# Performance work log

Hardware: AMD Instinct MI355X
Metric: run time of the kernel (lower is better)

## Reference

```python
import itertools
import jax, jax.numpy as jnp
import numpy as np

B = 1024      # graphs
N = 40        # atoms per graph (module supports 1..49)
ETA = 64
K = 32        # num_clusters
ZD = 32       # z_dim
NA = 10       # num_atom_types
NB = 5        # num_bond_types + 1
CH, AH, BH = 128, 128, 64
TAU = 1.0


def _resblock(x, W1, b1, W2, b2, Ws, bs):
    # assumed ResidualBlock: Linear->ReLU->(dropout, eval=identity)->Linear + linear skip
    h = jax.nn.relu(x @ W1 + b1)
    return h @ W2 + b2 + (x @ Ws + bs)


def setup_inputs() -> dict:
    key = jax.random.key(0)
    ks = jax.random.split(key, 24)
    s = 0.05
    pairs = np.array(list(itertools.combinations(range(N), 2)), dtype=np.int32)  # [780,2]
    offsets = (np.arange(B, dtype=np.int32) * N)[:, None, None]
    edge_index = jnp.asarray((pairs[None] + offsets).reshape(-1, 2))  # [B*780, 2]
    return {
        "eta": jax.random.normal(ks[0], (B, ETA), jnp.float32),
        "gumbel_noise": jax.random.gumbel(ks[1], (B * N, K), jnp.float32),
        "z_noise": jax.random.normal(ks[2], (B * N, ZD), jnp.float32),
        "cW1": jax.random.normal(ks[3], (ETA, CH)) * s, "cb1": jnp.zeros((CH,)),
        "cW2": jax.random.normal(ks[4], (CH, K)) * s, "cb2": jnp.zeros((K,)),
        "cWs": jax.random.normal(ks[5], (ETA, K)) * s, "cbs": jnp.zeros((K,)),
        "cluster_means": jax.random.normal(ks[6], (K, ZD)),
        "cluster_log_sigmas": jnp.full((K, ZD), -2.0),
        "aW1": jax.random.normal(ks[7], (ZD, AH)) * s, "ab1": jnp.zeros((AH,)),
        "aW2": jax.random.normal(ks[8], (AH, NA)) * s, "ab2": jnp.zeros((NA,)),
        "aWs": jax.random.normal(ks[9], (ZD, NA)) * s, "abs_": jnp.zeros((NA,)),
        "bond_matrix": jax.random.normal(ks[10], (NB, ZD, ZD)),
        "bW1": jax.random.normal(ks[11], (NB, BH)) * s, "bb1": jnp.zeros((BH,)),
        "bW2": jax.random.normal(ks[12], (BH, NB)) * s, "bb2": jnp.zeros((NB,)),
        "bWs": jax.random.normal(ks[13], (NB, NB)) * s, "bbs": jnp.zeros((NB,)),
        "edge_index": edge_index,
    }


def reference(eta, gumbel_noise, z_noise,
              cW1, cb1, cW2, cb2, cWs, cbs,
              cluster_means, cluster_log_sigmas,
              aW1, ab1, aW2, ab2, aWs, abs_,
              bond_matrix, bW1, bb1, bW2, bb2, bWs, bbs,
              edge_index):
    # decode_eta: mixture weights
    pi = jax.nn.softmax(_resblock(eta, cW1, cb1, cW2, cb2, cWs, cbs), axis=1)  # [B,K]
    log_pi = jnp.log(pi)
    # sample_c: gumbel-softmax (hard, straight-through) per node
    logits = jnp.repeat(log_pi, N, axis=0)                      # [B*N, K]
    y_soft = jax.nn.softmax((logits + gumbel_noise) / TAU, axis=-1)
    y_hard = jax.nn.one_hot(jnp.argmax(y_soft, axis=-1), K, dtype=y_soft.dtype)
    c = y_hard + y_soft - jax.lax.stop_gradient(y_soft)         # straight-through
    # sample_z
    mu = c @ cluster_means                                      # [B*N, ZD]
    log_sigma = c @ cluster_log_sigmas
    sigma = jnp.exp(jnp.clip(log_sigma, -20.0, 30.0))
    z = z_noise * sigma + mu
    # decode_z: atom logits
    atom_types = _resblock(z, aW1, ab1, aW2, ab2, aWs, abs_)    # [B*N, NA]
    # symmetrized per-bond-type bilinear form over edge node pairs
    Wsym = 0.5 * (bond_matrix + jnp.swapaxes(bond_matrix, 1, 2))  # [NB, ZD, ZD]
    zi = z[edge_index[:, 0]]                                    # [E, ZD]
    zj = z[edge_index[:, 1]]                                    # [E, ZD]
    bil = jnp.einsum('ed,tdc,ec->et', zi, Wsym, zj)             # [E, NB]
    edge_logits = _resblock(bil, bW1, bb1, bW2, bb2, bWs, bbs)
    edge_types = jax.nn.softmax(edge_logits, axis=1)            # [E, NB]
    return atom_types, edge_types
```

## Files before the change

kernel.cpp:

```cpp
#include <hip/hip_runtime.h>

constexpr int NPAIR = 780;

constexpr int OFF_ZT = 0;
constexpr int OFF_A  = 1280;
constexpr int UTP    = 1280;
constexpr int OFF_BT = 5120;
constexpr int SH_TOT = 9020;

__global__ __launch_bounds__(256) void prep_kernel(
    const float* __restrict__ eta,
    const float* __restrict__ cW1, const float* __restrict__ cb1,
    const float* __restrict__ cW2, const float* __restrict__ cb2,
    const float* __restrict__ cWs, const float* __restrict__ cbs,
    const float* __restrict__ bond, const float* __restrict__ lsig,
    const float* __restrict__ bW1, const float* __restrict__ bb1,
    const float* __restrict__ bW2, const float* __restrict__ bb2,
    const float* __restrict__ bWs, const float* __restrict__ bbs,
    float* __restrict__ log_pi, float* __restrict__ wsym,
    float* __restrict__ sigma, float* __restrict__ hwg)
{
  if (blockIdx.x < 256) {
    const int lane = threadIdx.x & 63, wid = threadIdx.x >> 6;
    const int row = blockIdx.x * 4 + wid;
    __shared__ __align__(16) float etas[4][64];
    __shared__ __align__(16) float hs[4][128];
    etas[wid][lane] = eta[row * 64 + lane];
    __syncthreads();
    float a0 = cb1[lane], a1 = cb1[lane + 64];
    for (int d = 0; d < 64; ++d) {
      float ed = etas[wid][d];
      a0 += ed * cW1[d * 128 + lane];
      a1 += ed * cW1[d * 128 + lane + 64];
    }
    hs[wid][lane] = fmaxf(a0, 0.f);
    hs[wid][lane + 64] = fmaxf(a1, 0.f);
    __syncthreads();
    if (lane < 32) {
      float x = cb2[lane] + cbs[lane];
      for (int j = 0; j < 128; ++j) x += hs[wid][j] * cW2[j * 32 + lane];
      for (int d = 0; d < 64; ++d) x += etas[wid][d] * cWs[d * 32 + lane];
      float m = x;
      for (int off = 16; off; off >>= 1) m = fmaxf(m, __shfl_xor(m, off));
      float e = __expf(x - m);
      float s = e;
      for (int off = 16; off; off >>= 1) s += __shfl_xor(s, off);
      log_pi[row * 32 + lane] = (x - m) - __logf(s);
    }
  } else {
    const int e = (blockIdx.x - 256) * 256 + threadIdx.x;
    if (e < 5120) {
      const int t = e >> 10, r = e & 1023, c = r >> 5, d = r & 31;
      wsym[e] = 0.5f * (bond[e] + bond[t * 1024 + d * 32 + c]);
    } else if (e < 6144) {
      const int q = e - 5120;
      sigma[q] = __expf(fminf(fmaxf(lsig[q], -20.f), 30.f));
    } else if (e < 6888) {
      const int idx = e - 6144;
      float v;
      if (idx < 320) v = bW1[idx];
      else if (idx < 384) v = bb1[idx - 320];
      else if (idx < 704) { int qq = idx - 384; int t2 = qq >> 6, j = qq & 63; v = bW2[j * 5 + t2]; }
      else if (idx < 709) v = bb2[idx - 704];
      else if (idx < 734) v = bWs[idx - 709];
      else v = bbs[idx - 734];
      hwg[idx] = v;
    }
  }
}

__global__ __launch_bounds__(256, 4) void fused_kernel(
    const float* __restrict__ log_pi, const float* __restrict__ gumbel,
    const float* __restrict__ z_noise,
    const float* __restrict__ means, const float* __restrict__ sigma,
    const float* __restrict__ aW1, const float* __restrict__ ab1,
    const float* __restrict__ aW2, const float* __restrict__ ab2,
    const float* __restrict__ aWs, const float* __restrict__ abs_,
    const float* __restrict__ wsym, const float* __restrict__ hwg,
    float* __restrict__ atom_out, float* __restrict__ edge_out)
{
  __shared__ __align__(16) float S[SH_TOT];
  const int tid = threadIdx.x;
  const int m = blockIdx.x;

  if (tid < 40) {
    const int n = m * 40 + tid;
    float lp[32];
    #pragma unroll
    for (int c = 0; c < 32; ++c) lp[c] = log_pi[m * 32 + c];
    float g[32];
    const float4* g4 = (const float4*)(gumbel + (size_t)n * 32);
    #pragma unroll
    for (int q = 0; q < 8; ++q) {
      float4 v = g4[q];
      g[4*q] = v.x; g[4*q+1] = v.y; g[4*q+2] = v.z; g[4*q+3] = v.w;
    }
    int kb = 0; float vb = lp[0] + g[0];
    #pragma unroll
    for (int c = 1; c < 32; ++c) {
      float v = lp[c] + g[c];
      if (v > vb) { vb = v; kb = c; }
    }
    const float4* zn4 = (const float4*)(z_noise + (size_t)n * 32);
    const float4* mk4 = (const float4*)(means + kb * 32);
    const float4* sg4 = (const float4*)(sigma + kb * 32);
    #pragma unroll
    for (int q = 0; q < 8; ++q) {
      float4 zn = zn4[q], mk = mk4[q], sg = sg4[q];
      S[OFF_ZT + (4*q    ) * 40 + tid] = zn.x * sg.x + mk.x;
      S[OFF_ZT + (4*q + 1) * 40 + tid] = zn.y * sg.y + mk.y;
      S[OFF_ZT + (4*q + 2) * 40 + tid] = zn.z * sg.z + mk.z;
      S[OFF_ZT + (4*q + 3) * 40 + tid] = zn.w * sg.w + mk.w;
    }
  }
  __syncthreads();

  for (int u = tid; u < 320; u += 256) {
    const int ng = u >> 5, jg = u & 31;
    const int n0 = ng * 4, j0 = jg * 4;
    float acc[4][4];
    #pragma unroll
    for (int a = 0; a < 4; ++a)
      #pragma unroll
      for (int b = 0; b < 4; ++b) acc[a][b] = 0.f;
    #pragma unroll 8
    for (int c = 0; c < 32; ++c) {
      float4 zv = *(const float4*)&S[OFF_ZT + c * 40 + n0];
      float4 wv = *(const float4*)(aW1 + c * 128 + j0);
      acc[0][0] += zv.x * wv.x; acc[0][1] += zv.x * wv.y; acc[0][2] += zv.x * wv.z; acc[0][3] += zv.x * wv.w;
      acc[1][0] += zv.y * wv.x; acc[1][1] += zv.y * wv.y; acc[1][2] += zv.y * wv.z; acc[1][3] += zv.y * wv.w;
      acc[2][0] += zv.z * wv.x; acc[2][1] += zv.z * wv.y; acc[2][2] += zv.z * wv.z; acc[2][3] += zv.z * wv.w;
      acc[3][0] += zv.w * wv.x; acc[3][1] += zv.w * wv.y; acc[3][2] += zv.w * wv.z; acc[3][3] += zv.w * wv.w;
    }
    float4 bv = *(const float4*)(ab1 + j0);
    #pragma unroll
    for (int a = 0; a < 4; ++a) {
      float4 hv;
      hv.x = fmaxf(acc[a][0] + bv.x, 0.f);
      hv.y = fmaxf(acc[a][1] + bv.y, 0.f);
      hv.z = fmaxf(acc[a][2] + bv.z, 0.f);
      hv.w = fmaxf(acc[a][3] + bv.w, 0.f);
      *(float4*)&S[OFF_A + (n0 + a) * 132 + j0] = hv;
    }
  }
  __syncthreads();

  if (tid < 200) {
    const int n = tid / 5, kp = tid - (tid / 5) * 5, k0 = kp * 2;
    float a0 = ab2[k0] + abs_[k0];
    float a1 = ab2[k0 + 1] + abs_[k0 + 1];
    #pragma unroll 8
    for (int c = 0; c < 32; ++c) {
      float zc = S[OFF_ZT + c * 40 + n];
      float2 w = *(const float2*)(aWs + c * 10 + k0);
      a0 += zc * w.x; a1 += zc * w.y;
    }
    #pragma unroll 8
    for (int j = 0; j < 128; ++j) {
      float hv = S[OFF_A + n * 132 + j];
      float2 w = *(const float2*)(aW2 + j * 10 + k0);
      a0 += hv * w.x; a1 += hv * w.y;
    }
    *(float2*)(atom_out + (size_t)m * 400 + n * 10 + k0) = make_float2(a0, a1);
  }
  __syncthreads();

  #pragma unroll
  for (int R = 0; R < 2; ++R) {
    const int tbase = (R == 0) ? 0 : 3;
    const int nplanes = (R == 0) ? 3 : 2;
    if (tid < nplanes * 80) {
      const int tl = tid / 80, r = tid - tl * 80;
      const int dg = r / 10, ig = r - dg * 10;
      const int d0 = dg * 4, i0 = ig * 4;
      const float* wg = wsym + (tbase + tl) * 1024;
      float acc[4][4];
      #pragma unroll
      for (int a = 0; a < 4; ++a)
        #pragma unroll
        for (int b = 0; b < 4; ++b) acc[a][b] = 0.f;
      #pragma unroll 8
      for (int c = 0; c < 32; ++c) {
        float4 zv = *(const float4*)&S[OFF_ZT + c * 40 + i0];
        float4 wv = *(const float4*)(wg + c * 32 + d0);
        acc[0][0] += wv.x * zv.x; acc[0][1] += wv.x * zv.y; acc[0][2] += wv.x * zv.z; acc[0][3] += wv.x * zv.w;
        acc[1][0] += wv.y * zv.x; acc[1][1] += wv.y * zv.y; acc[1][2] += wv.y * zv.z; acc[1][3] += wv.y * zv.w;
        acc[2][0] += wv.z * zv.x; acc[2][1] += wv.z * zv.y; acc[2][2] += wv.z * zv.z; acc[2][3] += wv.z * zv.w;
        acc[3][0] += wv.w * zv.x; acc[3][1] += wv.w * zv.y; acc[3][2] += wv.w * zv.z; acc[3][3] += wv.w * zv.w;
      }
      #pragma unroll
      for (int a = 0; a < 4; ++a)
        *(float4*)&S[OFF_A + tl * UTP + (d0 + a) * 40 + i0] =
            make_float4(acc[a][0], acc[a][1], acc[a][2], acc[a][3]);
    }
    __syncthreads();

    if (tid < nplanes * 55) {
      const int tl = tid / 55;
      int q = tid - tl * 55;
      int ig = 0;
      while (q >= 10 - ig) { q -= 10 - ig; ++ig; }
      const int jg = ig + q;
      const int i0 = ig * 4, j0 = jg * 4;
      float acc[4][4];
      #pragma unroll
      for (int a = 0; a < 4; ++a)
        #pragma unroll
        for (int b = 0; b < 4; ++b) acc[a][b] = 0.f;
      #pragma unroll 8
      for (int d = 0; d < 32; ++d) {
        float4 uv = *(const float4*)&S[OFF_A + tl * UTP + d * 40 + i0];
        float4 zv = *(const float4*)&S[OFF_ZT + d * 40 + j0];
        acc[0][0] += uv.x * zv.x; acc[0][1] += uv.x * zv.y; acc[0][2] += uv.x * zv.z; acc[0][3] += uv.x * zv.w;
        acc[1][0] += uv.y * zv.x; acc[1][1] += uv.y * zv.y; acc[1][2] += uv.y * zv.z; acc[1][3] += uv.y * zv.w;
        acc[2][0] += uv.z * zv.x; acc[2][1] += uv.z * zv.y; acc[2][2] += uv.z * zv.z; acc[2][3] += uv.z * zv.w;
        acc[3][0] += uv.w * zv.x; acc[3][1] += uv.w * zv.y; acc[3][2] += uv.w * zv.z; acc[3][3] += uv.w * zv.w;
      }
      const int tg = tbase + tl;
      #pragma unroll
      for (int a = 0; a < 4; ++a) {
        const int i = i0 + a;
        #pragma unroll
        for (int b = 0; b < 4; ++b) {
          const int j = j0 + b;
          if (i < j) {
            const int p = i * (79 - i) / 2 + (j - i - 1);
            S[OFF_BT + tg * 780 + p] = acc[a][b];
          }
        }
      }
    }
    __syncthreads();
  }

  const float* w1h = hwg;
  const float* b1h = hwg + 320;
  const float* w2t = hwg + 384;
  const float* b2h = hwg + 704;
  const float* wsh = hwg + 709;
  const float* bsh = hwg + 734;

  float bil5[3][5], lg[3][5];
  #pragma unroll
  for (int s = 0; s < 3; ++s) {
    const int p = tid + (s << 8);
    #pragma unroll
    for (int t = 0; t < 5; ++t) bil5[s][t] = S[OFF_BT + t * 780 + p];
    #pragma unroll
    for (int t2 = 0; t2 < 5; ++t2) {
      float a = b2h[t2] + bsh[t2];
      #pragma unroll
      for (int t = 0; t < 5; ++t) a += bil5[s][t] * wsh[t * 5 + t2];
      lg[s][t2] = a;
    }
  }
  for (int j4 = 0; j4 < 16; ++j4) {
    float4 bb = ((const float4*)b1h)[j4];
    float4 h[3];
    #pragma unroll
    for (int s = 0; s < 3; ++s) h[s] = bb;
    #pragma unroll
    for (int t = 0; t < 5; ++t) {
      float4 w1 = ((const float4*)(w1h + t * 64))[j4];
      #pragma unroll
      for (int s = 0; s < 3; ++s) {
        float bt = bil5[s][t];
        h[s].x += bt * w1.x; h[s].y += bt * w1.y; h[s].z += bt * w1.z; h[s].w += bt * w1.w;
      }
    }
    #pragma unroll
    for (int s = 0; s < 3; ++s) {
      h[s].x = fmaxf(h[s].x, 0.f); h[s].y = fmaxf(h[s].y, 0.f);
      h[s].z = fmaxf(h[s].z, 0.f); h[s].w = fmaxf(h[s].w, 0.f);
    }
    #pragma unroll
    for (int t2 = 0; t2 < 5; ++t2) {
      float4 w2 = ((const float4*)(w2t + t2 * 64))[j4];
      #pragma unroll
      for (int s = 0; s < 3; ++s)
        lg[s][t2] += h[s].x * w2.x + h[s].y * w2.y + h[s].z * w2.z + h[s].w * w2.w;
    }
  }
  #pragma unroll
  for (int s = 0; s < 3; ++s) {
    const int p = tid + (s << 8);
    float mx = lg[s][0];
    #pragma unroll
    for (int t2 = 1; t2 < 5; ++t2) mx = fmaxf(mx, lg[s][t2]);
    float e[5], sum = 0.f;
    #pragma unroll
    for (int t2 = 0; t2 < 5; ++t2) { e[t2] = __expf(lg[s][t2] - mx); sum += e[t2]; }
    float inv = 1.f / sum;
    float* outp = edge_out + ((size_t)m * NPAIR + p) * 5;
    #pragma unroll
    for (int t2 = 0; t2 < 5; ++t2) outp[t2] = e[t2] * inv;
  }

  if (tid < 12) {
    const int p = 768 + tid;
    float bt[5], lgt[5];
    #pragma unroll
    for (int t = 0; t < 5; ++t) bt[t] = S[OFF_BT + t * 780 + p];
    #pragma unroll
    for (int t2 = 0; t2 < 5; ++t2) {
      float a = b2h[t2] + bsh[t2];
      #pragma unroll
      for (int t = 0; t < 5; ++t) a += bt[t] * wsh[t * 5 + t2];
      lgt[t2] = a;
    }
    for (int j = 0; j < 64; ++j) {
      float hv = b1h[j];
      #pragma unroll
      for (int t = 0; t < 5; ++t) hv += bt[t] * w1h[t * 64 + j];
      hv = fmaxf(hv, 0.f);
      #pragma unroll
      for (int t2 = 0; t2 < 5; ++t2) lgt[t2] += hv * w2t[t2 * 64 + j];
    }
    float mx = lgt[0];
    #pragma unroll
    for (int t2 = 1; t2 < 5; ++t2) mx = fmaxf(mx, lgt[t2]);
    float e[5], sum = 0.f;
    #pragma unroll
    for (int t2 = 0; t2 < 5; ++t2) { e[t2] = __expf(lgt[t2] - mx); sum += e[t2]; }
    float inv = 1.f / sum;
    float* outp = edge_out + ((size_t)m * NPAIR + p) * 5;
    #pragma unroll
    for (int t2 = 0; t2 < 5; ++t2) outp[t2] = e[t2] * inv;
  }
}

extern "C" void kernel_launch(void* const* d_in, const int* in_sizes, int n_in,
                              void* d_out, int out_size, void* d_ws, size_t ws_size,
                              hipStream_t stream) {
  const float* eta    = (const float*)d_in[0];
  const float* gumbel = (const float*)d_in[1];
  const float* z_noise= (const float*)d_in[2];
  const float* cW1 = (const float*)d_in[3];
  const float* cb1 = (const float*)d_in[4];
  const float* cW2 = (const float*)d_in[5];
  const float* cb2 = (const float*)d_in[6];
  const float* cWs = (const float*)d_in[7];
  const float* cbs = (const float*)d_in[8];
  const float* means = (const float*)d_in[9];
  const float* lsig  = (const float*)d_in[10];
  const float* aW1 = (const float*)d_in[11];
  const float* ab1 = (const float*)d_in[12];
  const float* aW2 = (const float*)d_in[13];
  const float* ab2 = (const float*)d_in[14];
  const float* aWs = (const float*)d_in[15];
  const float* abs_= (const float*)d_in[16];
  const float* bond= (const float*)d_in[17];
  const float* bW1 = (const float*)d_in[18];
  const float* bb1 = (const float*)d_in[19];
  const float* bW2 = (const float*)d_in[20];
  const float* bb2 = (const float*)d_in[21];
  const float* bWs = (const float*)d_in[22];
  const float* bbs = (const float*)d_in[23];

  float* wsym   = (float*)d_ws;
  float* sigma  = wsym + 5120;
  float* hwg    = sigma + 1024;
  float* log_pi = hwg + 768;
  float* atom_out = (float*)d_out;
  float* edge_out = atom_out + (size_t)1024 * 400;

  prep_kernel<<<284, 256, 0, stream>>>(eta, cW1, cb1, cW2, cb2, cWs, cbs,
                                       bond, lsig, bW1, bb1, bW2, bb2, bWs, bbs,
                                       log_pi, wsym, sigma, hwg);
  fused_kernel<<<1024, 256, 0, stream>>>(log_pi, gumbel, z_noise,
                                         means, sigma, aW1, ab1, aW2, ab2, aWs, abs_,
                                         wsym, hwg, atom_out, edge_out);
}
```

Before: 183.0 us.

## Split z sampling into separate kernel writing transposed z buffer

Moves the Gumbel argmax and z sampling out of the fused per-graph kernel into a new z_kernel that processes 8 graphs per block with all 320 threads active, writing z in transposed layout to a workspace buffer. The fused kernel then just copies its 1280-float slice into shared memory. This removes the serial phase where only 40 of 256 threads worked while the rest waited at the barrier. The cost is an extra kernel launch and a global round trip for z.

```diff
diff --git a/kernel.cpp b/kernel.cpp
--- a/kernel.cpp
+++ b/kernel.cpp
@@ -69,10 +69,52 @@
   }
 }
 
-__global__ __launch_bounds__(256, 4) void fused_kernel(
+__global__ __launch_bounds__(320) void z_kernel(
     const float* __restrict__ log_pi, const float* __restrict__ gumbel,
     const float* __restrict__ z_noise,
     const float* __restrict__ means, const float* __restrict__ sigma,
+    float* __restrict__ zbufT)
+{
+  __shared__ float lps[256];
+  const int tid = threadIdx.x;
+  const int m0 = blockIdx.x * 8;
+  if (tid < 256) lps[tid] = log_pi[m0 * 32 + tid];
+  __syncthreads();
+
+  const int n = blockIdx.x * 320 + tid;
+  const int ml = tid / 40;
+  const int nn = tid - ml * 40;
+  const float* lp = &lps[ml * 32];
+
+  float g[32];
+  const float4* g4 = (const float4*)(gumbel + (size_t)n * 32);
+  #pragma unroll
+  for (int q = 0; q < 8; ++q) {
+    float4 v = g4[q];
+    g[4*q] = v.x; g[4*q+1] = v.y; g[4*q+2] = v.z; g[4*q+3] = v.w;
+  }
+  int kb = 0; float vb = lp[0] + g[0];
+  #pragma unroll
+  for (int c = 1; c < 32; ++c) {
+    float v = lp[c] + g[c];
+    if (v > vb) { vb = v; kb = c; }
+  }
+  const float4* zn4 = (const float4*)(z_noise + (size_t)n * 32);
+  const float4* mk4 = (const float4*)(means + kb * 32);
+  const float4* sg4 = (const float4*)(sigma + kb * 32);
+  float* zt = zbufT + (size_t)(m0 + ml) * 1280 + nn;
+  #pragma unroll
+  for (int q = 0; q < 8; ++q) {
+    float4 zn = zn4[q], mk = mk4[q], sg = sg4[q];
+    zt[(4*q    ) * 40] = zn.x * sg.x + mk.x;
+    zt[(4*q + 1) * 40] = zn.y * sg.y + mk.y;
+    zt[(4*q + 2) * 40] = zn.z * sg.z + mk.z;
+    zt[(4*q + 3) * 40] = zn.w * sg.w + mk.w;
+  }
+}
+
+__global__ __launch_bounds__(256, 4) void fused_kernel(
+    const float* __restrict__ zbufT,
     const float* __restrict__ aW1, const float* __restrict__ ab1,
     const float* __restrict__ aW2, const float* __restrict__ ab2,
     const float* __restrict__ aWs, const float* __restrict__ abs_,
@@ -83,35 +125,10 @@
   const int tid = threadIdx.x;
   const int m = blockIdx.x;
 
-  if (tid < 40) {
-    const int n = m * 40 + tid;
-    float lp[32];
-    #pragma unroll
-    for (int c = 0; c < 32; ++c) lp[c] = log_pi[m * 32 + c];
-    float g[32];
-    const float4* g4 = (const float4*)(gumbel + (size_t)n * 32);
-    #pragma unroll
-    for (int q = 0; q < 8; ++q) {
-      float4 v = g4[q];
-      g[4*q] = v.x; g[4*q+1] = v.y; g[4*q+2] = v.z; g[4*q+3] = v.w;
-    }
-    int kb = 0; float vb = lp[0] + g[0];
-    #pragma unroll
-    for (int c = 1; c < 32; ++c) {
-      float v = lp[c] + g[c];
-      if (v > vb) { vb = v; kb = c; }
-    }
-    const float4* zn4 = (const float4*)(z_noise + (size_t)n * 32);
-    const float4* mk4 = (const float4*)(means + kb * 32);
-    const float4* sg4 = (const float4*)(sigma + kb * 32);
-    #pragma unroll
-    for (int q = 0; q < 8; ++q) {
-      float4 zn = zn4[q], mk = mk4[q], sg = sg4[q];
-      S[OFF_ZT + (4*q    ) * 40 + tid] = zn.x * sg.x + mk.x;
-      S[OFF_ZT + (4*q + 1) * 40 + tid] = zn.y * sg.y + mk.y;
-      S[OFF_ZT + (4*q + 2) * 40 + tid] = zn.z * sg.z + mk.z;
-      S[OFF_ZT + (4*q + 3) * 40 + tid] = zn.w * sg.w + mk.w;
-    }
+  {
+    const float4* src = (const float4*)(zbufT + (size_t)m * 1280);
+    for (int u = tid; u < 320; u += 256)
+      *(float4*)&S[OFF_ZT + u * 4] = src[u];
   }
   __syncthreads();
 
@@ -361,13 +378,14 @@
   float* sigma  = wsym + 5120;
   float* hwg    = sigma + 1024;
   float* log_pi = hwg + 768;
+  float* zbufT  = log_pi + 32768;
   float* atom_out = (float*)d_out;
   float* edge_out = atom_out + (size_t)1024 * 400;
 
   prep_kernel<<<284, 256, 0, stream>>>(eta, cW1, cb1, cW2, cb2, cWs, cbs,
                                        bond, lsig, bW1, bb1, bW2, bb2, bWs, bbs,
                                        log_pi, wsym, sigma, hwg);
-  fused_kernel<<<1024, 256, 0, stream>>>(log_pi, gumbel, z_noise,
-                                         means, sigma, aW1, ab1, aW2, ab2, aWs, abs_,
+  z_kernel<<<128, 320, 0, stream>>>(log_pi, gumbel, z_noise, means, sigma, zbufT);
+  fused_kernel<<<1024, 256, 0, stream>>>(zbufT, aW1, ab1, aW2, ab2, aWs, abs_,
                                          wsym, hwg, atom_out, edge_out);
 }
```

Result: slower. 187.7 us (+2.6%).
